# Optimization experiments

Hardware: AMD Instinct MI355X
Metric: run time of the kernel (lower is better)

Reference implementation:

```python
import jax, jax.numpy as jnp
import numpy as np

N_HEAD = 8
LN_EPS = 1e-6


def setup_inputs() -> dict:
    key = jax.random.key(0)
    ks = jax.random.split(key, 6)
    B, S, D = 4, 2048, 256  # D = hidden_size*2 = input_dim
    sc = 1.0 / np.sqrt(D)
    return {
        "inputs": jax.random.normal(ks[0], (B, S, D), jnp.float32),
        "Wq": jax.random.normal(ks[1], (D, D), jnp.float32) * sc,
        "Wk": jax.random.normal(ks[2], (D, D), jnp.float32) * sc,
        "Wv": jax.random.normal(ks[3], (D, D), jnp.float32) * sc,
        "Wf": jax.random.normal(ks[4], (D, D), jnp.float32) * sc,
        "bf": jnp.zeros((D,), jnp.float32),
        "gamma": jnp.ones((D,), jnp.float32),
        "beta": jnp.zeros((D,), jnp.float32),
    }


def reference(inputs, Wq, Wk, Wv, Wf, bf, gamma, beta):
    B, S, D = inputs.shape
    H = N_HEAD
    dh = D // H
    # Projections (torch Linear: x @ W.T), no bias for Q/K/V
    Q = (inputs @ Wq.T).reshape(B, S, H, dh)
    K = (inputs @ Wk.T).reshape(B, S, H, dh)
    V = (inputs @ Wv.T).reshape(B, S, H, dh)
    # NOTE: original scales by sqrt(K.shape[1]) == sqrt(seq_len), not sqrt(dh)
    scale = 1.0 / jnp.sqrt(jnp.float32(S)).astype(inputs.dtype)
    scores = jnp.einsum("bqhd,bkhd->bhqk", Q, K) * scale  # [B,H,S,S]
    attn = jax.nn.softmax(scores, axis=-1)
    out = jnp.einsum("bhqk,bkhd->bqhd", attn, V).reshape(B, S, D)
    out = out @ Wf.T + bf
    # residual + LayerNorm(eps=1e-6)
    x = inputs + out
    mu = jnp.mean(x, axis=-1, keepdims=True)
    var = jnp.mean(jnp.square(x - mu), axis=-1, keepdims=True)
    return (x - mu) * jax.lax.rsqrt(var + LN_EPS) * gamma + beta
```

## Files before the change

### kernel.cpp

```cpp
#include <hip/hip_runtime.h>
#include <hip/hip_bf16.h>

typedef __attribute__((ext_vector_type(8))) short short8;
typedef __attribute__((ext_vector_type(4))) float f32x4;
typedef __attribute__((ext_vector_type(16))) float f32x16;

#define DEVI __device__ __forceinline__

DEVI unsigned short f2bf(float f) {
  union { float f; unsigned int u; } v; v.f = f;
  unsigned int r = v.u + 0x7fffu + ((v.u >> 16) & 1u);
  return (unsigned short)(r >> 16);
}

DEVI unsigned int cvt2(float lo, float hi) {
  unsigned int r;
  asm("v_cvt_pk_bf16_f32 %0, %1, %2" : "=v"(r) : "v"(lo), "v"(hi));
  return r;
}

#define GLDS16(gp, lp)                                                         \
  __builtin_amdgcn_global_load_lds(                                            \
      (const __attribute__((address_space(1))) unsigned int*)(uintptr_t)(gp),  \
      (__attribute__((address_space(3))) unsigned int*)(uintptr_t)(lp), 16, 0, 0)

#define SB 4
#define SS 2048
#define SD 256
#define SH 8
#define SDH 32
#define SM 8192

#define QSCALE 0.0318793654f

#define Q_OFF   0
#define K_OFF   (SM * SD)
#define VT_OFF  (2 * SM * SD)
#define AO_OFF  (3 * SM * SD)

__global__ __launch_bounds__(256) void qkv_k(
    const float* __restrict__ X, const float* __restrict__ Wq,
    const float* __restrict__ Wk, const float* __restrict__ Wv,
    unsigned short* __restrict__ ws) {
  __shared__ __align__(16) unsigned short Atile[128][72];
  __shared__ __align__(16) unsigned short Btile[128][72];
  int tid = threadIdx.x, w = tid >> 6, lane = tid & 63, g = lane >> 4, r = lane & 15;
  int m0 = blockIdx.x * 128, n0 = blockIdx.y * 128;
  int z = n0 >> 8, nbase = n0 & 255;
  const float* Wz = (z == 0) ? Wq : (z == 1) ? Wk : Wv;
  int wr = (w >> 1) * 64, wc = (w & 1) * 64;
  f32x4 acc[4][4] = {};
  int srow = tid >> 3, scol = (tid & 7) * 8;
  float4 a0[4], a1[4], b0[4], b1[4];
#pragma unroll
  for (int p = 0; p < 4; ++p) {
    const float* xa = X + (m0 + srow + p * 32) * SD + scol;
    const float* xb = Wz + (nbase + srow + p * 32) * SD + scol;
    a0[p] = *reinterpret_cast<const float4*>(xa);
    a1[p] = *reinterpret_cast<const float4*>(xa + 4);
    b0[p] = *reinterpret_cast<const float4*>(xb);
    b1[p] = *reinterpret_cast<const float4*>(xb + 4);
  }
  for (int k0 = 0; k0 < SD; k0 += 64) {
    __syncthreads();
#pragma unroll
    for (int p = 0; p < 4; ++p) {
      uint4 ua = { cvt2(a0[p].x, a0[p].y), cvt2(a0[p].z, a0[p].w),
                   cvt2(a1[p].x, a1[p].y), cvt2(a1[p].z, a1[p].w) };
      uint4 ub = { cvt2(b0[p].x, b0[p].y), cvt2(b0[p].z, b0[p].w),
                   cvt2(b1[p].x, b1[p].y), cvt2(b1[p].z, b1[p].w) };
      *reinterpret_cast<uint4*>(&Atile[srow + p * 32][scol]) = ua;
      *reinterpret_cast<uint4*>(&Btile[srow + p * 32][scol]) = ub;
    }
    __syncthreads();
    if (k0 + 64 < SD) {
#pragma unroll
      for (int p = 0; p < 4; ++p) {
        const float* xa = X + (m0 + srow + p * 32) * SD + k0 + 64 + scol;
        const float* xb = Wz + (nbase + srow + p * 32) * SD + k0 + 64 + scol;
        a0[p] = *reinterpret_cast<const float4*>(xa);
        a1[p] = *reinterpret_cast<const float4*>(xa + 4);
        b0[p] = *reinterpret_cast<const float4*>(xb);
        b1[p] = *reinterpret_cast<const float4*>(xb + 4);
      }
    }
#pragma unroll
    for (int ks = 0; ks < 2; ++ks) {
      short8 af[4], bf[4];
#pragma unroll
      for (int i = 0; i < 4; ++i)
        af[i] = *reinterpret_cast<const short8*>(&Atile[wr + i * 16 + r][ks * 32 + g * 8]);
#pragma unroll
      for (int j = 0; j < 4; ++j)
        bf[j] = *reinterpret_cast<const short8*>(&Btile[wc + j * 16 + r][ks * 32 + g * 8]);
#pragma unroll
      for (int i = 0; i < 4; ++i)
#pragma unroll
        for (int j = 0; j < 4; ++j)
          acc[i][j] = __builtin_amdgcn_mfma_f32_16x16x32_bf16(af[i], bf[j], acc[i][j], 0, 0, 0);
    }
  }
  int b_ = m0 >> 11, sbase = m0 & 2047;
  float qs = (z == 0) ? QSCALE : 1.0f;
  unsigned short* Vt = &Btile[0][0];
#pragma unroll
  for (int p = 0; p < 2; ++p) {
    __syncthreads();
    if ((w & 1) == p) {
      if (z < 2) {
#pragma unroll
        for (int i = 0; i < 4; ++i)
#pragma unroll
          for (int j = 0; j < 4; ++j)
#pragma unroll
            for (int jj = 0; jj < 4; ++jj)
              Atile[wr + i * 16 + g * 4 + jj][j * 16 + r] = f2bf(acc[i][j][jj] * qs);
      } else {
#pragma unroll
        for (int i = 0; i < 4; ++i)
#pragma unroll
          for (int j = 0; j < 4; ++j) {
            unsigned short o4[4];
#pragma unroll
            for (int jj = 0; jj < 4; ++jj) o4[jj] = f2bf(acc[i][j][jj]);
            *reinterpret_cast<uint2*>(&Vt[(j * 16 + r) * 136 + wr + i * 16 + g * 4]) =
                *reinterpret_cast<const uint2*>(o4);
          }
      }
    }
    __syncthreads();
    if (z < 2) {
      unsigned short* out = ws + (z == 0 ? Q_OFF : K_OFF);
      int h0 = (nbase + p * 64) >> 5;
#pragma unroll
      for (int it = 0; it < 4; ++it) {
        int c = it * 256 + tid;
        int m = c >> 3, cr = c & 7, hl = cr >> 2, ch = cr & 3;
        short8 val = *reinterpret_cast<const short8*>(&Atile[m][hl * 32 + ch * 8]);
        int h = h0 + hl;
        *reinterpret_cast<short8*>(
            out + (((b_ << 3) + h) * SS + sbase + m) * SDH + ch * 8) = val;
      }
    } else {
      unsigned short* out = ws + VT_OFF;
      int nb = nbase + p * 64;
#pragma unroll
      for (int it = 0; it < 4; ++it) {
        int c = it * 256 + tid;
        int nl = c >> 4, ch = c & 15;
        short8 val = *reinterpret_cast<const short8*>(&Vt[nl * 136 + ch * 8]);
        int col = nb + nl, h = col >> 5, d = col & 31;
        *reinterpret_cast<short8*>(
            out + ((((b_ << 3) + h) << 5) + d) * SS + sbase + ch * 8) = val;
      }
    }
  }
}

__global__ __launch_bounds__(512, 4) void attn_k(const unsigned short* __restrict__ ws_c,
                                                 unsigned short* __restrict__ ws) {
  __shared__ __align__(16) unsigned char smem[65536];
  int tid = threadIdx.x, w = tid >> 6, lane = tid & 63;
  int wg = w >> 2, wl = w & 3, gtid = tid & 255;
  int n32 = lane & 31, hi = lane >> 5;
  int wgid = ((blockIdx.x & 7) << 6) + (blockIdx.x >> 3);
  int bh = wgid >> 4, qb = wgid & 15;
  int q0 = qb * 128 + wl * 32;
  const unsigned short* Qh = ws_c + Q_OFF + bh * (SS * SDH);
  const unsigned short* Kg = ws_c + K_OFF + (bh * SS + wg * 1024) * SDH;
  const unsigned short* Vg = ws_c + VT_OFF + bh * (SDH * SS) + wg * 1024;
  short8 qB0 = *reinterpret_cast<const short8*>(Qh + (q0 + n32) * SDH + 8 * hi);
  short8 qB1 = *reinterpret_cast<const short8*>(Qh + (q0 + n32) * SDH + 16 + 8 * hi);
  unsigned short* Kbuf0 = (unsigned short*)(smem + wg * 16384);
  unsigned short* Kbuf1 = (unsigned short*)(smem + wg * 16384 + 8192);
  unsigned short* Vbuf0 = (unsigned short*)(smem + 32768 + wg * 16384);
  unsigned short* Vbuf1 = (unsigned short*)(smem + 32768 + wg * 16384 + 8192);
  int wv = gtid >> 6;
  int kr = gtid >> 2;
  int kcg = (gtid & 3) ^ ((kr >> 1) & 3);
  const unsigned short* gK0 = Kg + kr * SDH + kcg * 8;
  const unsigned short* gK1 = gK0 + 64 * SDH;
  int vr = gtid >> 4;
  int vcg = (gtid & 15) ^ (vr & 7);
  const unsigned short* gV0 = Vg + vr * SS + vcg * 8;
  const unsigned short* gV1 = gV0 + 16 * SS;
  auto issue = [&](int buf, int tt) {
    char* kd = (char*)(buf ? Kbuf1 : Kbuf0) + wv * 1024;
    char* vd = (char*)(buf ? Vbuf1 : Vbuf0) + wv * 1024;
    GLDS16(gK0 + tt * 4096, kd);
    GLDS16(gK1 + tt * 4096, kd + 4096);
    GLDS16(gV0 + tt * 128, vd);
    GLDS16(gV1 + tt * 128, vd + 4096);
  };
  issue(0, 0);
  f32x16 O = {}, Lf = {};
  union { unsigned int u[4]; short8 sv; } ONES;
  ONES.u[0] = 0x3F803F80u; ONES.u[1] = 0x3F803F80u;
  ONES.u[2] = 0x3F803F80u; ONES.u[3] = 0x3F803F80u;
  int rb = (n32 >> 1) & 3;
  int koff0 = (hi ^ rb) * 8;
  int koff1 = ((2 + hi) ^ rb) * 8;
  int vb7 = n32 & 7;
  for (int t = 0; t < 8; ++t) {
    const unsigned short* Kt = (t & 1) ? Kbuf1 : Kbuf0;
    const unsigned short* Vt = (t & 1) ? Vbuf1 : Vbuf0;
    if (t < 7) {
      issue((t + 1) & 1, t + 1);
      asm volatile("s_waitcnt vmcnt(4)" ::: "memory");
    } else {
      asm volatile("s_waitcnt vmcnt(0)" ::: "memory");
    }
    __builtin_amdgcn_s_barrier();
    f32x16 aC = {}, aN = {};
    {
      const unsigned short* krow = Kt + n32 * 32;
      short8 ka = *reinterpret_cast<const short8*>(krow + koff0);
      short8 kb = *reinterpret_cast<const short8*>(krow + koff1);
      aC = __builtin_amdgcn_mfma_f32_32x32x16_bf16(ka, qB0, aC, 0, 0, 0);
      aC = __builtin_amdgcn_mfma_f32_32x32x16_bf16(kb, qB1, aC, 0, 0, 0);
    }
#pragma unroll
    for (int s = 0; s < 4; ++s) {
      if (s < 3) {
        const unsigned short* krow = Kt + ((s + 1) * 32 + n32) * 32;
        short8 ka = *reinterpret_cast<const short8*>(krow + koff0);
        short8 kb = *reinterpret_cast<const short8*>(krow + koff1);
        f32x16 z = {};
        z = __builtin_amdgcn_mfma_f32_32x32x16_bf16(ka, qB0, z, 0, 0, 0);
        z = __builtin_amdgcn_mfma_f32_32x32x16_bf16(kb, qB1, z, 0, 0, 0);
        aN = z;
      }
#pragma unroll
      for (int i = 0; i < 16; ++i) aC[i] = __builtin_amdgcn_exp2f(aC[i]);
      unsigned int pk[8];
#pragma unroll
      for (int i = 0; i < 8; ++i) pk[i] = cvt2(aC[2 * i], aC[2 * i + 1]);
      asm("v_permlane32_swap_b32 %0, %1" : "+v"(pk[0]), "+v"(pk[2]));
      asm("v_permlane32_swap_b32 %0, %1" : "+v"(pk[1]), "+v"(pk[3]));
      asm("v_permlane32_swap_b32 %0, %1" : "+v"(pk[4]), "+v"(pk[6]));
      asm("v_permlane32_swap_b32 %0, %1" : "+v"(pk[5]), "+v"(pk[7]));
      union { unsigned int u[4]; short8 sv; } A1, A2;
      A1.u[0] = pk[0]; A1.u[1] = pk[1]; A1.u[2] = pk[2]; A1.u[3] = pk[3];
      A2.u[0] = pk[4]; A2.u[1] = pk[5]; A2.u[2] = pk[6]; A2.u[3] = pk[7];
      const unsigned short* vrow = Vt + n32 * 128;
      short8 vB0 = *reinterpret_cast<const short8*>(vrow + ((s * 4 + hi) ^ vb7) * 8);
      short8 vB1 = *reinterpret_cast<const short8*>(vrow + ((s * 4 + 2 + hi) ^ vb7) * 8);
      O  = __builtin_amdgcn_mfma_f32_32x32x16_bf16(A1.sv, vB0, O, 0, 0, 0);
      O  = __builtin_amdgcn_mfma_f32_32x32x16_bf16(A2.sv, vB1, O, 0, 0, 0);
      Lf = __builtin_amdgcn_mfma_f32_32x32x16_bf16(A1.sv, ONES.sv, Lf, 0, 0, 0);
      Lf = __builtin_amdgcn_mfma_f32_32x32x16_bf16(A2.sv, ONES.sv, Lf, 0, 0, 0);
      if (s < 3) aC = aN;
    }
    __builtin_amdgcn_s_barrier();
  }
  __syncthreads();
  float* OCf = reinterpret_cast<float*>(smem);
  float* LCf = OCf + 16 * 257;
  int p = wl * 64 + lane;
  if (wg == 1) {
#pragma unroll
    for (int i = 0; i < 16; ++i) { OCf[i * 257 + p] = O[i]; LCf[i * 257 + p] = Lf[i]; }
  }
  __syncthreads();
  if (wg == 0) {
    int b = bh >> 3, h = bh & 7;
    unsigned short* AO = ws + AO_OFF;
#pragma unroll
    for (int rr = 0; rr < 16; ++rr) {
      float Ot = O[rr] + OCf[rr * 257 + p];
      float Lt = Lf[rr] + LCf[rr * 257 + p];
      int q = (rr & 3) + 8 * (rr >> 2) + 4 * hi;
      AO[(b * SS + q0 + q) * SD + h * SDH + n32] = f2bf(Ot / Lt);
    }
  }
}

__global__ __launch_bounds__(256) void final_k(
    const unsigned short* __restrict__ ws_c, const float* __restrict__ X,
    const float* __restrict__ Wf, const float* __restrict__ bfv,
    const float* __restrict__ gamma, const float* __restrict__ beta,
    float* __restrict__ out) {
  __shared__ __align__(16) unsigned short Al[32][72];
  __shared__ __align__(16) unsigned short Bl[256][72];
  __shared__ float Cl[32][257];
  const unsigned short* AO = ws_c + AO_OFF;
  int tid = threadIdx.x, w = tid >> 6, lane = tid & 63, g = lane >> 4, r = lane & 15;
  int m0 = blockIdx.x * 32;
  f32x4 acc[2][4] = {};
  int arow = tid >> 3, acol = (tid & 7) * 8;
  for (int k0 = 0; k0 < SD; k0 += 64) {
    short8 av = *reinterpret_cast<const short8*>(AO + (m0 + arow) * SD + k0 + acol);
    float4 w0[8], w1[8];
#pragma unroll
    for (int i = 0; i < 8; i++) {
      const float* wp = Wf + (i * 32 + arow) * SD + k0 + acol;
      w0[i] = *reinterpret_cast<const float4*>(wp);
      w1[i] = *reinterpret_cast<const float4*>(wp + 4);
    }
    __syncthreads();
    *reinterpret_cast<short8*>(&Al[arow][acol]) = av;
#pragma unroll
    for (int i = 0; i < 8; i++) {
      uint4 ub = { cvt2(w0[i].x, w0[i].y), cvt2(w0[i].z, w0[i].w),
                   cvt2(w1[i].x, w1[i].y), cvt2(w1[i].z, w1[i].w) };
      *reinterpret_cast<uint4*>(&Bl[i * 32 + arow][acol]) = ub;
    }
    __syncthreads();
#pragma unroll
    for (int ks = 0; ks < 2; ks++) {
      short8 af0 = *reinterpret_cast<const short8*>(&Al[r][ks * 32 + g * 8]);
      short8 af1 = *reinterpret_cast<const short8*>(&Al[16 + r][ks * 32 + g * 8]);
#pragma unroll
      for (int nt = 0; nt < 4; nt++) {
        short8 bb = *reinterpret_cast<const short8*>(&Bl[w * 64 + nt * 16 + r][ks * 32 + g * 8]);
        acc[0][nt] = __builtin_amdgcn_mfma_f32_16x16x32_bf16(af0, bb, acc[0][nt], 0, 0, 0);
        acc[1][nt] = __builtin_amdgcn_mfma_f32_16x16x32_bf16(af1, bb, acc[1][nt], 0, 0, 0);
      }
    }
  }
#pragma unroll
  for (int rt = 0; rt < 2; rt++)
#pragma unroll
    for (int nt = 0; nt < 4; nt++)
#pragma unroll
      for (int j = 0; j < 4; j++)
        Cl[rt * 16 + g * 4 + j][w * 64 + nt * 16 + r] = acc[rt][nt][j];
  __syncthreads();
  int row = tid >> 3, sub = tid & 7;
  int m = m0 + row;
  float x[32];
  float sum = 0.f, sumsq = 0.f;
#pragma unroll
  for (int i = 0; i < 8; i++) {
    int col = sub * 32 + i * 4;
    float4 xv = *reinterpret_cast<const float4*>(X + m * SD + col);
    float4 bb = *reinterpret_cast<const float4*>(bfv + col);
    x[i * 4 + 0] = Cl[row][col + 0] + xv.x + bb.x;
    x[i * 4 + 1] = Cl[row][col + 1] + xv.y + bb.y;
    x[i * 4 + 2] = Cl[row][col + 2] + xv.z + bb.z;
    x[i * 4 + 3] = Cl[row][col + 3] + xv.w + bb.w;
  }
#pragma unroll
  for (int c = 0; c < 32; c++) { sum += x[c]; sumsq += x[c] * x[c]; }
  sum += __shfl_xor(sum, 1);  sumsq += __shfl_xor(sumsq, 1);
  sum += __shfl_xor(sum, 2);  sumsq += __shfl_xor(sumsq, 2);
  sum += __shfl_xor(sum, 4);  sumsq += __shfl_xor(sumsq, 4);
  float mean = sum * (1.0f / 256.0f);
  float var = sumsq * (1.0f / 256.0f) - mean * mean;
  float rstd = rsqrtf(var + 1e-6f);
#pragma unroll
  for (int i = 0; i < 8; i++) {
    int col = sub * 32 + i * 4;
    float4 gv = *reinterpret_cast<const float4*>(gamma + col);
    float4 bv2 = *reinterpret_cast<const float4*>(beta + col);
    float4 ov;
    ov.x = (x[i * 4 + 0] - mean) * rstd * gv.x + bv2.x;
    ov.y = (x[i * 4 + 1] - mean) * rstd * gv.y + bv2.y;
    ov.z = (x[i * 4 + 2] - mean) * rstd * gv.z + bv2.z;
    ov.w = (x[i * 4 + 3] - mean) * rstd * gv.w + bv2.w;
    *reinterpret_cast<float4*>(out + m * SD + col) = ov;
  }
}

extern "C" void kernel_launch(void* const* d_in, const int* in_sizes, int n_in,
                              void* d_out, int out_size, void* d_ws, size_t ws_size,
                              hipStream_t stream) {
  const float* X  = (const float*)d_in[0];
  const float* Wq = (const float*)d_in[1];
  const float* Wk = (const float*)d_in[2];
  const float* Wv = (const float*)d_in[3];
  const float* Wf = (const float*)d_in[4];
  const float* bf = (const float*)d_in[5];
  const float* gm = (const float*)d_in[6];
  const float* bt = (const float*)d_in[7];
  float* out = (float*)d_out;
  unsigned short* ws = (unsigned short*)d_ws;

  qkv_k<<<dim3(64, 6), 256, 0, stream>>>(X, Wq, Wk, Wv, ws);
  attn_k<<<dim3(512), 512, 0, stream>>>(ws, ws);
  final_k<<<256, 256, 0, stream>>>(ws, X, Wf, bf, gm, bt, out);
}
```

Baseline: 58.97 us.

## Split attention KV range across two blocks, merge partial sums in final kernel

After: 64.57 us. 1.09x slower.

```diff
diff --git a/kernel.cpp b/kernel.cpp
--- a/kernel.cpp
+++ b/kernel.cpp
@@ -36,7 +36,8 @@
 #define Q_OFF   0
 #define K_OFF   (SM * SD)
 #define VT_OFF  (2 * SM * SD)
-#define AO_OFF  (3 * SM * SD)
+#define OPF     3145728
+#define LPF     (OPF + 2 * SM * SD)
 
 __global__ __launch_bounds__(256) void qkv_k(
     const float* __restrict__ X, const float* __restrict__ Wq,
@@ -157,40 +158,30 @@
   }
 }
 
-__global__ __launch_bounds__(512, 4) void attn_k(const unsigned short* __restrict__ ws_c,
+__global__ __launch_bounds__(512, 6) void attn_k(const unsigned short* __restrict__ ws_c,
                                                  unsigned short* __restrict__ ws) {
-  __shared__ __align__(16) unsigned char smem[65536];
+  __shared__ __align__(16) unsigned char smem[32768];
   int tid = threadIdx.x, w = tid >> 6, lane = tid & 63;
   int wg = w >> 2, wl = w & 3, gtid = tid & 255;
   int n32 = lane & 31, hi = lane >> 5;
-  int wgid = ((blockIdx.x & 7) << 6) + (blockIdx.x >> 3);
-  int bh = wgid >> 4, qb = wgid & 15;
+  int wgid = ((blockIdx.x & 7) << 7) + (blockIdx.x >> 3);
+  int bh = wgid >> 5, qb = (wgid >> 1) & 15, kvh = wgid & 1;
   int q0 = qb * 128 + wl * 32;
   const unsigned short* Qh = ws_c + Q_OFF + bh * (SS * SDH);
-  const unsigned short* Kg = ws_c + K_OFF + (bh * SS + wg * 1024) * SDH;
-  const unsigned short* Vg = ws_c + VT_OFF + bh * (SDH * SS) + wg * 1024;
+  const unsigned short* Kg = ws_c + K_OFF + (bh * SS + kvh * 1024 + wg * 512) * SDH;
+  const unsigned short* Vg = ws_c + VT_OFF + bh * (SDH * SS) + kvh * 1024 + wg * 512;
   short8 qB0 = *reinterpret_cast<const short8*>(Qh + (q0 + n32) * SDH + 8 * hi);
   short8 qB1 = *reinterpret_cast<const short8*>(Qh + (q0 + n32) * SDH + 16 + 8 * hi);
-  unsigned short* Kbuf0 = (unsigned short*)(smem + wg * 16384);
-  unsigned short* Kbuf1 = (unsigned short*)(smem + wg * 16384 + 8192);
-  unsigned short* Vbuf0 = (unsigned short*)(smem + 32768 + wg * 16384);
-  unsigned short* Vbuf1 = (unsigned short*)(smem + 32768 + wg * 16384 + 8192);
+  int kr = gtid >> 2, kcg = (gtid & 3) ^ ((kr >> 1) & 3);
+  const unsigned short* gK = Kg + kr * SDH + kcg * 8;
+  int vr = gtid >> 3, vcg = (gtid & 7) ^ (vr & 7);
+  const unsigned short* gV = Vg + vr * SS + vcg * 8;
   int wv = gtid >> 6;
-  int kr = gtid >> 2;
-  int kcg = (gtid & 3) ^ ((kr >> 1) & 3);
-  const unsigned short* gK0 = Kg + kr * SDH + kcg * 8;
-  const unsigned short* gK1 = gK0 + 64 * SDH;
-  int vr = gtid >> 4;
-  int vcg = (gtid & 15) ^ (vr & 7);
-  const unsigned short* gV0 = Vg + vr * SS + vcg * 8;
-  const unsigned short* gV1 = gV0 + 16 * SS;
   auto issue = [&](int buf, int tt) {
-    char* kd = (char*)(buf ? Kbuf1 : Kbuf0) + wv * 1024;
-    char* vd = (char*)(buf ? Vbuf1 : Vbuf0) + wv * 1024;
-    GLDS16(gK0 + tt * 4096, kd);
-    GLDS16(gK1 + tt * 4096, kd + 4096);
-    GLDS16(gV0 + tt * 128, vd);
-    GLDS16(gV1 + tt * 128, vd + 4096);
+    char* kd = (char*)smem + wg * 8192 + buf * 4096 + wv * 1024;
+    char* vd = (char*)smem + 16384 + wg * 8192 + buf * 4096 + wv * 1024;
+    GLDS16(gK + tt * 2048, kd);
+    GLDS16(gV + tt * 64, vd);
   };
   issue(0, 0);
   f32x16 O = {}, Lf = {};
@@ -202,34 +193,25 @@
   int koff1 = ((2 + hi) ^ rb) * 8;
   int vb7 = n32 & 7;
   for (int t = 0; t < 8; ++t) {
-    const unsigned short* Kt = (t & 1) ? Kbuf1 : Kbuf0;
-    const unsigned short* Vt = (t & 1) ? Vbuf1 : Vbuf0;
+    const unsigned short* Kt = (const unsigned short*)(smem + wg * 8192 + (t & 1) * 4096);
+    const unsigned short* Vt = (const unsigned short*)(smem + 16384 + wg * 8192 + (t & 1) * 4096);
     if (t < 7) {
       issue((t + 1) & 1, t + 1);
-      asm volatile("s_waitcnt vmcnt(4)" ::: "memory");
+      asm volatile("s_waitcnt vmcnt(2)" ::: "memory");
     } else {
       asm volatile("s_waitcnt vmcnt(0)" ::: "memory");
     }
     __builtin_amdgcn_s_barrier();
-    f32x16 aC = {}, aN = {};
-    {
-      const unsigned short* krow = Kt + n32 * 32;
+#pragma unroll
+    for (int s = 0; s < 2; ++s) {
+      const unsigned short* krow = Kt + (s * 32 + n32) * 32;
       short8 ka = *reinterpret_cast<const short8*>(krow + koff0);
       short8 kb = *reinterpret_cast<const short8*>(krow + koff1);
+      f32x16 aC = {};
+      __builtin_amdgcn_s_setprio(1);
       aC = __builtin_amdgcn_mfma_f32_32x32x16_bf16(ka, qB0, aC, 0, 0, 0);
       aC = __builtin_amdgcn_mfma_f32_32x32x16_bf16(kb, qB1, aC, 0, 0, 0);
-    }
-#pragma unroll
-    for (int s = 0; s < 4; ++s) {
-      if (s < 3) {
-        const unsigned short* krow = Kt + ((s + 1) * 32 + n32) * 32;
-        short8 ka = *reinterpret_cast<const short8*>(krow + koff0);
-        short8 kb = *reinterpret_cast<const short8*>(krow + koff1);
-        f32x16 z = {};
-        z = __builtin_amdgcn_mfma_f32_32x32x16_bf16(ka, qB0, z, 0, 0, 0);
-        z = __builtin_amdgcn_mfma_f32_32x32x16_bf16(kb, qB1, z, 0, 0, 0);
-        aN = z;
-      }
+      __builtin_amdgcn_s_setprio(0);
 #pragma unroll
       for (int i = 0; i < 16; ++i) aC[i] = __builtin_amdgcn_exp2f(aC[i]);
       unsigned int pk[8];
@@ -242,14 +224,15 @@
       union { unsigned int u[4]; short8 sv; } A1, A2;
       A1.u[0] = pk[0]; A1.u[1] = pk[1]; A1.u[2] = pk[2]; A1.u[3] = pk[3];
       A2.u[0] = pk[4]; A2.u[1] = pk[5]; A2.u[2] = pk[6]; A2.u[3] = pk[7];
-      const unsigned short* vrow = Vt + n32 * 128;
+      const unsigned short* vrow = Vt + n32 * 64;
       short8 vB0 = *reinterpret_cast<const short8*>(vrow + ((s * 4 + hi) ^ vb7) * 8);
       short8 vB1 = *reinterpret_cast<const short8*>(vrow + ((s * 4 + 2 + hi) ^ vb7) * 8);
+      __builtin_amdgcn_s_setprio(1);
       O  = __builtin_amdgcn_mfma_f32_32x32x16_bf16(A1.sv, vB0, O, 0, 0, 0);
       O  = __builtin_amdgcn_mfma_f32_32x32x16_bf16(A2.sv, vB1, O, 0, 0, 0);
       Lf = __builtin_amdgcn_mfma_f32_32x32x16_bf16(A1.sv, ONES.sv, Lf, 0, 0, 0);
       Lf = __builtin_amdgcn_mfma_f32_32x32x16_bf16(A2.sv, ONES.sv, Lf, 0, 0, 0);
-      if (s < 3) aC = aN;
+      __builtin_amdgcn_s_setprio(0);
     }
     __builtin_amdgcn_s_barrier();
   }
@@ -259,18 +242,26 @@
   int p = wl * 64 + lane;
   if (wg == 1) {
 #pragma unroll
-    for (int i = 0; i < 16; ++i) { OCf[i * 257 + p] = O[i]; LCf[i * 257 + p] = Lf[i]; }
+    for (int i = 0; i < 16; ++i) {
+      OCf[i * 257 + p] = O[i];
+      if (n32 == 0) {
+        int q = (i & 3) + 8 * (i >> 2) + 4 * hi;
+        LCf[wl * 32 + q] = Lf[i];
+      }
+    }
   }
   __syncthreads();
   if (wg == 0) {
     int b = bh >> 3, h = bh & 7;
-    unsigned short* AO = ws + AO_OFF;
+    float* OPp = (float*)ws + OPF + (size_t)kvh * (SM * SD);
+    float* LPp = (float*)ws + LPF + (size_t)kvh * (32 * SS) + bh * SS;
 #pragma unroll
     for (int rr = 0; rr < 16; ++rr) {
+      int q = (rr & 3) + 8 * (rr >> 2) + 4 * hi;
       float Ot = O[rr] + OCf[rr * 257 + p];
-      float Lt = Lf[rr] + LCf[rr * 257 + p];
-      int q = (rr & 3) + 8 * (rr >> 2) + 4 * hi;
-      AO[(b * SS + q0 + q) * SD + h * SDH + n32] = f2bf(Ot / Lt);
+      float Lt = Lf[rr] + LCf[wl * 32 + q];
+      OPp[(b * SS + q0 + q) * SD + h * SDH + n32] = Ot;
+      if (n32 == 0) LPp[q0 + q] = Lt;
     }
   }
 }
@@ -283,13 +274,30 @@
   __shared__ __align__(16) unsigned short Al[32][72];
   __shared__ __align__(16) unsigned short Bl[256][72];
   __shared__ float Cl[32][257];
-  const unsigned short* AO = ws_c + AO_OFF;
+  const float* OP0 = (const float*)ws_c + OPF;
+  const float* OP1 = OP0 + (SM * SD);
+  const float* LP0 = (const float*)ws_c + LPF;
+  const float* LP1 = LP0 + (32 * SS);
   int tid = threadIdx.x, w = tid >> 6, lane = tid & 63, g = lane >> 4, r = lane & 15;
   int m0 = blockIdx.x * 32;
   f32x4 acc[2][4] = {};
   int arow = tid >> 3, acol = (tid & 7) * 8;
+  int m = m0 + arow, b_ = m >> 11, s2 = m & 2047;
   for (int k0 = 0; k0 < SD; k0 += 64) {
-    short8 av = *reinterpret_cast<const short8*>(AO + (m0 + arow) * SD + k0 + acol);
+    int col0 = k0 + acol;
+    int h = col0 >> 5;
+    float Ls = LP0[(b_ * 8 + h) * SS + s2] + LP1[(b_ * 8 + h) * SS + s2];
+    float inv = 1.0f / Ls;
+    const float* p0 = OP0 + (size_t)m * SD + col0;
+    const float* p1 = OP1 + (size_t)m * SD + col0;
+    float4 x0 = *reinterpret_cast<const float4*>(p0);
+    float4 x1 = *reinterpret_cast<const float4*>(p0 + 4);
+    float4 y0 = *reinterpret_cast<const float4*>(p1);
+    float4 y1 = *reinterpret_cast<const float4*>(p1 + 4);
+    uint4 av = { cvt2((x0.x + y0.x) * inv, (x0.y + y0.y) * inv),
+                 cvt2((x0.z + y0.z) * inv, (x0.w + y0.w) * inv),
+                 cvt2((x1.x + y1.x) * inv, (x1.y + y1.y) * inv),
+                 cvt2((x1.z + y1.z) * inv, (x1.w + y1.w) * inv) };
     float4 w0[8], w1[8];
 #pragma unroll
     for (int i = 0; i < 8; i++) {
@@ -298,7 +306,7 @@
       w1[i] = *reinterpret_cast<const float4*>(wp + 4);
     }
     __syncthreads();
-    *reinterpret_cast<short8*>(&Al[arow][acol]) = av;
+    *reinterpret_cast<uint4*>(&Al[arow][acol]) = av;
 #pragma unroll
     for (int i = 0; i < 8; i++) {
       uint4 ub = { cvt2(w0[i].x, w0[i].y), cvt2(w0[i].z, w0[i].w),
@@ -327,13 +335,13 @@
         Cl[rt * 16 + g * 4 + j][w * 64 + nt * 16 + r] = acc[rt][nt][j];
   __syncthreads();
   int row = tid >> 3, sub = tid & 7;
-  int m = m0 + row;
+  int mm = m0 + row;
   float x[32];
   float sum = 0.f, sumsq = 0.f;
 #pragma unroll
   for (int i = 0; i < 8; i++) {
     int col = sub * 32 + i * 4;
-    float4 xv = *reinterpret_cast<const float4*>(X + m * SD + col);
+    float4 xv = *reinterpret_cast<const float4*>(X + mm * SD + col);
     float4 bb = *reinterpret_cast<const float4*>(bfv + col);
     x[i * 4 + 0] = Cl[row][col + 0] + xv.x + bb.x;
     x[i * 4 + 1] = Cl[row][col + 1] + xv.y + bb.y;
@@ -358,7 +366,7 @@
     ov.y = (x[i * 4 + 1] - mean) * rstd * gv.y + bv2.y;
     ov.z = (x[i * 4 + 2] - mean) * rstd * gv.z + bv2.z;
     ov.w = (x[i * 4 + 3] - mean) * rstd * gv.w + bv2.w;
-    *reinterpret_cast<float4*>(out + m * SD + col) = ov;
+    *reinterpret_cast<float4*>(out + mm * SD + col) = ov;
   }
 }
 
@@ -377,6 +385,6 @@
   unsigned short* ws = (unsigned short*)d_ws;
 
   qkv_k<<<dim3(64, 6), 256, 0, stream>>>(X, Wq, Wk, Wv, ws);
-  attn_k<<<dim3(512), 512, 0, stream>>>(ws, ws);
+  attn_k<<<dim3(1024), 512, 0, stream>>>(ws, ws);
   final_k<<<256, 256, 0, stream>>>(ws, X, Wf, bf, gm, bt, out);
 }
```
